# Kernel tuning notes

Hardware: AMD Instinct MI355X
Metric: run time of the kernel (lower is better)

The kernel has to match this reference:

```python
import jax, jax.numpy as jnp
import numpy as np

N_QUBITS = 6      # 4 data + 2 ancilla
N_DATA = 4
N_LAYERS = 4
N_GROUPS = 8
DIM = 2 ** N_QUBITS  # 64 statevector amplitudes (real: RY + CNOT keep state real)
GN_GROUPS = 32
EPS = 1e-5


def _cnot_ring_perm():
    # CNOT(q, q+1 mod n) ring applied sequentially; compose into one basis permutation.
    n = N_QUBITS
    f = np.arange(DIM)
    for c in range(n):
        t = (c + 1) % n
        cbit = (f >> (n - 1 - c)) & 1
        f = np.where(cbit == 1, f ^ (1 << (n - 1 - t)), f)
    # new_state[f[i]] = old_state[i]  =>  new = old[finv]
    finv = np.empty(DIM, dtype=np.int64)
    finv[f] = np.arange(DIM)
    return jnp.asarray(finv)


def _zsign():
    i = np.arange(DIM)[:, None]
    q = np.arange(N_DATA)[None, :]
    return jnp.asarray(1.0 - 2.0 * ((i >> (N_QUBITS - 1 - q)) & 1), dtype=jnp.float32)


PERM = _cnot_ring_perm()
ZSIGN = _zsign()


def _group_norm(x, gamma, beta):
    B, C, H, W = x.shape
    xg = x.reshape(B, GN_GROUPS, C // GN_GROUPS, H, W)
    mu = xg.mean(axis=(2, 3, 4), keepdims=True)
    var = xg.var(axis=(2, 3, 4), keepdims=True)
    xn = ((xg - mu) * jax.lax.rsqrt(var + EPS)).reshape(B, C, H, W)
    return xn * gamma[None, :, None, None] + beta[None, :, None, None]


def _apply_ry(state, half_angle, q):
    # state: [B,H,W,G,64]; half_angle: [B,H,W,G]; RY = [[c,-s],[s,c]] on qubit q
    pre, post = 2 ** q, 2 ** (N_QUBITS - 1 - q)
    s = state.reshape(state.shape[:-1] + (pre, 2, post))
    c = jnp.cos(half_angle)[..., None, None]
    sn = jnp.sin(half_angle)[..., None, None]
    a0, a1 = s[..., 0, :], s[..., 1, :]
    new = jnp.stack([c * a0 - sn * a1, sn * a0 + c * a1], axis=-2)
    return new.reshape(state.shape)


def _forward(x, emb, gamma, beta, w_in, b_in, theta, w_style, b_style, w_out, b_out):
    B, C, H, W = x.shape
    h = _group_norm(x, gamma, beta)                       # norm0
    emb_a = emb * jax.nn.sigmoid(emb)                     # SiLU(emb)
    # 1x1 projection to per-group data-qubit rotation angles: [B,H,W,G,4]
    ang = jnp.einsum('oc,bchw->bohw', w_in, h) + b_in[None, :, None, None]
    ang = ang.reshape(B, N_GROUPS, N_DATA, H, W).transpose(0, 3, 4, 1, 2)
    # style modulation of circuit parameters: [B,G,L,Q]
    style = (emb_a @ w_style.T + b_style).reshape(B, N_GROUPS, N_LAYERS, N_QUBITS)
    # init |0...0> per pixel per group
    state = jnp.zeros((B, H, W, N_GROUPS, DIM), x.dtype).at[..., 0].set(1.0)
    for l in range(N_LAYERS):
        for q in range(N_QUBITS):
            a = theta[:, l, q][None, None, None, :] + style[:, :, l, q][:, None, None, :]
            if q < N_DATA:                                # data reuploading each layer
                a = a + ang[..., q]
            state = _apply_ry(state, 0.5 * a, q)
        state = state[..., PERM]                          # CNOT ring entangler
    probs = state * state
    meas = probs @ ZSIGN                                  # [B,H,W,G,4] <Z> on data qubits
    meas = meas.transpose(0, 3, 4, 1, 2).reshape(B, N_GROUPS * N_DATA, H, W)
    out = jnp.einsum('oc,bchw->bohw', w_out, meas) + b_out[None, :, None, None]
    return out + x                                        # residual


def setup_inputs() -> dict:
    key = jax.random.key(0)
    ks = jax.random.split(key, 6)
    B, C, H, W, E = 16, 256, 32, 32, 512
    return {
        'x': jax.random.normal(ks[0], (B, C, H, W), jnp.float32),
        'emb': jax.random.normal(ks[1], (B, E), jnp.float32),
        'gamma': jnp.ones((C,), jnp.float32),
        'beta': jnp.zeros((C,), jnp.float32),
        'w_in': jax.random.normal(ks[2], (32, C), jnp.float32) * 0.1,
        'b_in': jnp.zeros((32,), jnp.float32),
        'theta': jax.random.normal(ks[3], (N_GROUPS, N_LAYERS, N_QUBITS), jnp.float32) * 0.5,
        'w_style': jax.random.normal(ks[4], (N_GROUPS * N_LAYERS * N_QUBITS, E), jnp.float32) * 0.02,
        'b_style': jnp.zeros((N_GROUPS * N_LAYERS * N_QUBITS,), jnp.float32),
        'w_out': jax.random.normal(ks[5], (C, 32), jnp.float32) * 0.05,
        'b_out': jnp.zeros((C,), jnp.float32),
    }


def reference(x, emb, gamma, beta, w_in, b_in, theta, w_style, b_style, w_out, b_out):
    return _forward(x, emb, gamma, beta, w_in, b_in, theta, w_style, b_style, w_out, b_out)
```

## Files before the change

kernel.cpp:

```cpp
#include <hip/hip_runtime.h>
#include <math.h>

#define NB 16
#define NC 256
#define NHW 1024
#define NE 512
#define NGQ 8
#define NDQ 4
#define NLQ 4
#define NQB 6
#define QDIM 64
#define PIX 32
#define XS_STRIDE 36

struct PermT { int v[QDIM]; };
constexpr PermT make_perm() {
    PermT P{};
    int f[QDIM] = {};
    for (int i = 0; i < QDIM; ++i) f[i] = i;
    for (int c = 0; c < NQB; ++c) {
        int t = (c + 1) % NQB;
        for (int i = 0; i < QDIM; ++i)
            if ((f[i] >> (NQB - 1 - c)) & 1) f[i] ^= 1 << (NQB - 1 - t);
    }
    for (int i = 0; i < QDIM; ++i) P.v[f[i]] = i;
    return P;
}
constexpr PermT PERM = make_perm();

__global__ __launch_bounds__(256) void k_stats(const float* __restrict__ x,
                                               float* __restrict__ mu,
                                               float* __restrict__ rs) {
    int bg = blockIdx.x;
    const float4* xp = (const float4*)(x + (size_t)bg * 8 * NHW);
    float s = 0.f, ss = 0.f;
    for (int i = threadIdx.x; i < 8 * NHW / 4; i += 256) {
        float4 v = xp[i];
        s  += v.x + v.y + v.z + v.w;
        ss += v.x*v.x + v.y*v.y + v.z*v.z + v.w*v.w;
    }
    __shared__ float red0[4], red1[4];
    #pragma unroll
    for (int o = 32; o; o >>= 1) { s += __shfl_down(s, o); ss += __shfl_down(ss, o); }
    int lane = threadIdx.x & 63, w = threadIdx.x >> 6;
    if (lane == 0) { red0[w] = s; red1[w] = ss; }
    __syncthreads();
    if (threadIdx.x == 0) {
        s  = red0[0] + red0[1] + red0[2] + red0[3];
        ss = red1[0] + red1[1] + red1[2] + red1[3];
        float m = s * (1.f / 8192.f);
        float var = ss * (1.f / 8192.f) - m * m;
        mu[bg] = m;
        rs[bg] = rsqrtf(var + 1e-5f);
    }
}

__global__ __launch_bounds__(256) void k_style(const float* __restrict__ emb,
                                               const float* __restrict__ w_style,
                                               const float* __restrict__ b_style,
                                               const float* __restrict__ theta,
                                               float* __restrict__ A) {
    int b = blockIdx.x;
    __shared__ float es[NE];
    int t = threadIdx.x;
    for (int i = t; i < NE; i += 256) {
        float v = emb[b * NE + i];
        es[i] = v / (1.f + __expf(-v));
    }
    __syncthreads();
    int j0 = t >> 3, sub = t & 7;
    for (int pass = 0; pass < 6; ++pass) {
        int j = pass * 32 + j0;
        const float* wr = w_style + (size_t)j * NE + sub * 64;
        const float* er = es + sub * 64;
        float acc = 0.f;
        #pragma unroll
        for (int i = 0; i < 64; i += 4) {
            float4 w4 = *(const float4*)(wr + i);
            acc = fmaf(w4.x, er[i],   acc);
            acc = fmaf(w4.y, er[i+1], acc);
            acc = fmaf(w4.z, er[i+2], acc);
            acc = fmaf(w4.w, er[i+3], acc);
        }
        acc += __shfl_xor(acc, 1);
        acc += __shfl_xor(acc, 2);
        acc += __shfl_xor(acc, 4);
        if (sub == 0) A[b * 192 + j] = theta[j] + b_style[j] + acc;
    }
}

__global__ __launch_bounds__(256, 2) void k_main(const float* __restrict__ x,
                                                 const float* __restrict__ gamma,
                                                 const float* __restrict__ beta,
                                                 const float* __restrict__ w_in,
                                                 const float* __restrict__ b_in,
                                                 const float* __restrict__ A,
                                                 const float* __restrict__ w_out,
                                                 const float* __restrict__ b_out,
                                                 const float* __restrict__ mu,
                                                 const float* __restrict__ rs,
                                                 float* __restrict__ out) {
    __shared__ float xs[NC * XS_STRIDE];
    __shared__ float as_[32 * 32];
    __shared__ float ms[32 * 32];

    int blk = blockIdx.x;
    int b = blk >> 5;
    int pbase = (blk & 31) * PIX;
    int t = threadIdx.x;

    {
        int c0 = t >> 3, f4 = (t & 7) * 4;
        #pragma unroll
        for (int k = 0; k < 8; ++k) {
            int c = c0 + 32 * k;
            int gidx = b * 32 + (c >> 3);
            float m = mu[gidx], r = rs[gidx];
            float sc = r * gamma[c];
            float sh = beta[c] - m * sc;
            float4 x4 = *(const float4*)(x + (size_t)(b * NC + c) * NHW + pbase + f4);
            float4 h4;
            h4.x = fmaf(x4.x, sc, sh);
            h4.y = fmaf(x4.y, sc, sh);
            h4.z = fmaf(x4.z, sc, sh);
            h4.w = fmaf(x4.w, sc, sh);
            *(float4*)(xs + c * XS_STRIDE + f4) = h4;
        }
    }
    __syncthreads();

    {
        int o = t >> 3, f4 = (t & 7) * 4;
        const float* wr = w_in + o * NC;
        float4 acc = {0.f, 0.f, 0.f, 0.f};
        #pragma unroll 4
        for (int c = 0; c < NC; c += 4) {
            float4 w4 = *(const float4*)(wr + c);
            const float* xc = xs + c * XS_STRIDE + f4;
            float4 h0 = *(const float4*)(xc);
            float4 h1 = *(const float4*)(xc + XS_STRIDE);
            float4 h2 = *(const float4*)(xc + 2 * XS_STRIDE);
            float4 h3 = *(const float4*)(xc + 3 * XS_STRIDE);
            acc.x = fmaf(w4.x, h0.x, fmaf(w4.y, h1.x, fmaf(w4.z, h2.x, fmaf(w4.w, h3.x, acc.x))));
            acc.y = fmaf(w4.x, h0.y, fmaf(w4.y, h1.y, fmaf(w4.z, h2.y, fmaf(w4.w, h3.y, acc.y))));
            acc.z = fmaf(w4.x, h0.z, fmaf(w4.y, h1.z, fmaf(w4.z, h2.z, fmaf(w4.w, h3.z, acc.z))));
            acc.w = fmaf(w4.x, h0.w, fmaf(w4.y, h1.w, fmaf(w4.z, h2.w, fmaf(w4.w, h3.w, acc.w))));
        }
        float bi = b_in[o];
        float4 r = {acc.x + bi, acc.y + bi, acc.z + bi, acc.w + bi};
        *(float4*)(as_ + o * 32 + f4) = r;
    }
    __syncthreads();

    {
        int p = t & 31, g = t >> 5;
        float angp[NDQ];
        #pragma unroll
        for (int d = 0; d < NDQ; ++d) angp[d] = as_[(g * NDQ + d) * 32 + p];
        const float* Ab = A + b * 192 + g * 24;

        float st[QDIM];
        #pragma unroll
        for (int i = 0; i < QDIM; ++i) st[i] = 0.f;
        st[0] = 1.f;

        #pragma unroll
        for (int l = 0; l < NLQ; ++l) {
            #pragma unroll
            for (int q = 0; q < NQB; ++q) {
                float a = Ab[l * NQB + q] + (q < NDQ ? angp[q] : 0.f);
                float sn, cs;
                __sincosf(0.5f * a, &sn, &cs);
                const int m = 32 >> q;
                #pragma unroll
                for (int i = 0; i < QDIM; ++i) {
                    if (i & m) continue;
                    float a0 = st[i], a1 = st[i | m];
                    st[i]     = cs * a0 - sn * a1;
                    st[i | m] = sn * a0 + cs * a1;
                }
            }
            float tmp[QDIM];
            #pragma unroll
            for (int i = 0; i < QDIM; ++i) tmp[i] = st[PERM.v[i]];
            #pragma unroll
            for (int i = 0; i < QDIM; ++i) st[i] = tmp[i];
        }

        float pr[QDIM];
        #pragma unroll
        for (int i = 0; i < QDIM; ++i) pr[i] = st[i] * st[i];
        #pragma unroll
        for (int d = 0; d < NDQ; ++d) {
            const int mb = 32 >> d;
            float acc = 0.f;
            #pragma unroll
            for (int i = 0; i < QDIM; ++i) acc += (i & mb) ? -pr[i] : pr[i];
            ms[(g * NDQ + d) * 32 + p] = acc;
        }
    }
    __syncthreads();

    {
        int c0 = t >> 3, f4 = (t & 7) * 4;
        #pragma unroll
        for (int k = 0; k < 8; ++k) {
            int c = c0 + 32 * k;
            const float* wr = w_out + c * 32;
            float4 acc = {0.f, 0.f, 0.f, 0.f};
            #pragma unroll
            for (int o = 0; o < 32; o += 4) {
                float4 w4 = *(const float4*)(wr + o);
                const float* mc = ms + o * 32 + f4;
                float4 m0 = *(const float4*)(mc);
                float4 m1 = *(const float4*)(mc + 32);
                float4 m2 = *(const float4*)(mc + 64);
                float4 m3 = *(const float4*)(mc + 96);
                acc.x = fmaf(w4.x, m0.x, fmaf(w4.y, m1.x, fmaf(w4.z, m2.x, fmaf(w4.w, m3.x, acc.x))));
                acc.y = fmaf(w4.x, m0.y, fmaf(w4.y, m1.y, fmaf(w4.z, m2.y, fmaf(w4.w, m3.y, acc.y))));
                acc.z = fmaf(w4.x, m0.z, fmaf(w4.y, m1.z, fmaf(w4.z, m2.z, fmaf(w4.w, m3.z, acc.z))));
                acc.w = fmaf(w4.x, m0.w, fmaf(w4.y, m1.w, fmaf(w4.z, m2.w, fmaf(w4.w, m3.w, acc.w))));
            }
            size_t gidx = (size_t)(b * NC + c) * NHW + pbase + f4;
            float4 x4 = *(const float4*)(x + gidx);
            float bo = b_out[c];
            float4 r;
            r.x = acc.x + bo + x4.x;
            r.y = acc.y + bo + x4.y;
            r.z = acc.z + bo + x4.z;
            r.w = acc.w + bo + x4.w;
            *(float4*)(out + gidx) = r;
        }
    }
}

extern "C" void kernel_launch(void* const* d_in, const int* in_sizes, int n_in,
                              void* d_out, int out_size, void* d_ws, size_t ws_size,
                              hipStream_t stream) {
    const float* x       = (const float*)d_in[0];
    const float* emb     = (const float*)d_in[1];
    const float* gamma   = (const float*)d_in[2];
    const float* beta    = (const float*)d_in[3];
    const float* w_in    = (const float*)d_in[4];
    const float* b_in    = (const float*)d_in[5];
    const float* theta   = (const float*)d_in[6];
    const float* w_style = (const float*)d_in[7];
    const float* b_style = (const float*)d_in[8];
    const float* w_out   = (const float*)d_in[9];
    const float* b_out   = (const float*)d_in[10];
    float* out = (float*)d_out;

    float* ws = (float*)d_ws;
    float* mu = ws;
    float* rs = ws + 512;
    float* A  = ws + 1024;

    k_stats<<<NB * 32, 256, 0, stream>>>(x, mu, rs);
    k_style<<<NB, 256, 0, stream>>>(emb, w_style, b_style, theta, A);
    k_main<<<NB * 32, 256, 0, stream>>>(x, gamma, beta, w_in, b_in, A,
                                        w_out, b_out, mu, rs, out);
}
```

Before: 141.6 us.

## Transpose shared tiles to pixel-major and pack statevector math into float2 ops

Shared-memory activations are stored pixel-major, so each thread owns one pixel and streams weights as wave-uniform loads in both 1x1 projections. The statevector update is rewritten with two-wide vectors so the compiler can emit packed FMA instructions, and the last-qubit rotation becomes an in-pair swizzle. The measurement reduction is simplified, and the output stage now writes scalar coalesced values per pixel instead of float4. The risks are the scalar global stores and loads in the output stage, and possible LDS bank conflicts from the transposed stores in the normalization stage.

```diff
diff --git a/kernel.cpp b/kernel.cpp
--- a/kernel.cpp
+++ b/kernel.cpp
@@ -5,13 +5,15 @@
 #define NC 256
 #define NHW 1024
 #define NE 512
-#define NGQ 8
 #define NDQ 4
 #define NLQ 4
 #define NQB 6
 #define QDIM 64
 #define PIX 32
-#define XS_STRIDE 36
+#define XPAD 260
+#define MPAD 36
+
+typedef float v2f __attribute__((ext_vector_type(2)));
 
 struct PermT { int v[QDIM]; };
 constexpr PermT make_perm() {
@@ -89,6 +91,8 @@
     }
 }
 
+#define ELEM(arr, j) (((j) & 1) ? arr[(j) >> 1].y : arr[(j) >> 1].x)
+
 __global__ __launch_bounds__(256, 2) void k_main(const float* __restrict__ x,
                                                  const float* __restrict__ gamma,
                                                  const float* __restrict__ beta,
@@ -100,9 +104,9 @@
                                                  const float* __restrict__ mu,
                                                  const float* __restrict__ rs,
                                                  float* __restrict__ out) {
-    __shared__ float xs[NC * XS_STRIDE];
-    __shared__ float as_[32 * 32];
-    __shared__ float ms[32 * 32];
+    __shared__ float xs[PIX * XPAD];
+    __shared__ float as_[PIX * MPAD];
+    __shared__ float ms[PIX * MPAD];
 
     int blk = blockIdx.x;
     int b = blk >> 5;
@@ -119,117 +123,139 @@
             float sc = r * gamma[c];
             float sh = beta[c] - m * sc;
             float4 x4 = *(const float4*)(x + (size_t)(b * NC + c) * NHW + pbase + f4);
-            float4 h4;
-            h4.x = fmaf(x4.x, sc, sh);
-            h4.y = fmaf(x4.y, sc, sh);
-            h4.z = fmaf(x4.z, sc, sh);
-            h4.w = fmaf(x4.w, sc, sh);
-            *(float4*)(xs + c * XS_STRIDE + f4) = h4;
-        }
-    }
-    __syncthreads();
-
-    {
-        int o = t >> 3, f4 = (t & 7) * 4;
-        const float* wr = w_in + o * NC;
-        float4 acc = {0.f, 0.f, 0.f, 0.f};
-        #pragma unroll 4
+            xs[(f4 + 0) * XPAD + c] = fmaf(x4.x, sc, sh);
+            xs[(f4 + 1) * XPAD + c] = fmaf(x4.y, sc, sh);
+            xs[(f4 + 2) * XPAD + c] = fmaf(x4.z, sc, sh);
+            xs[(f4 + 3) * XPAD + c] = fmaf(x4.w, sc, sh);
+        }
+    }
+    __syncthreads();
+
+    {
+        int og = t >> 5, p = t & 31;
+        const float* wbase = w_in + og * 4 * NC;
+        const float* hrow = xs + p * XPAD;
+        float a0 = 0.f, a1 = 0.f, a2 = 0.f, a3 = 0.f;
+        #pragma unroll 8
         for (int c = 0; c < NC; c += 4) {
-            float4 w4 = *(const float4*)(wr + c);
-            const float* xc = xs + c * XS_STRIDE + f4;
-            float4 h0 = *(const float4*)(xc);
-            float4 h1 = *(const float4*)(xc + XS_STRIDE);
-            float4 h2 = *(const float4*)(xc + 2 * XS_STRIDE);
-            float4 h3 = *(const float4*)(xc + 3 * XS_STRIDE);
-            acc.x = fmaf(w4.x, h0.x, fmaf(w4.y, h1.x, fmaf(w4.z, h2.x, fmaf(w4.w, h3.x, acc.x))));
-            acc.y = fmaf(w4.x, h0.y, fmaf(w4.y, h1.y, fmaf(w4.z, h2.y, fmaf(w4.w, h3.y, acc.y))));
-            acc.z = fmaf(w4.x, h0.z, fmaf(w4.y, h1.z, fmaf(w4.z, h2.z, fmaf(w4.w, h3.z, acc.z))));
-            acc.w = fmaf(w4.x, h0.w, fmaf(w4.y, h1.w, fmaf(w4.z, h2.w, fmaf(w4.w, h3.w, acc.w))));
-        }
-        float bi = b_in[o];
-        float4 r = {acc.x + bi, acc.y + bi, acc.z + bi, acc.w + bi};
-        *(float4*)(as_ + o * 32 + f4) = r;
-    }
-    __syncthreads();
-
-    {
-        int p = t & 31, g = t >> 5;
-        float angp[NDQ];
-        #pragma unroll
-        for (int d = 0; d < NDQ; ++d) angp[d] = as_[(g * NDQ + d) * 32 + p];
+            float4 h = *(const float4*)(hrow + c);
+            float4 w0 = *(const float4*)(wbase + c);
+            float4 w1 = *(const float4*)(wbase + NC + c);
+            float4 w2 = *(const float4*)(wbase + 2 * NC + c);
+            float4 w3 = *(const float4*)(wbase + 3 * NC + c);
+            a0 = fmaf(w0.x, h.x, fmaf(w0.y, h.y, fmaf(w0.z, h.z, fmaf(w0.w, h.w, a0))));
+            a1 = fmaf(w1.x, h.x, fmaf(w1.y, h.y, fmaf(w1.z, h.z, fmaf(w1.w, h.w, a1))));
+            a2 = fmaf(w2.x, h.x, fmaf(w2.y, h.y, fmaf(w2.z, h.z, fmaf(w2.w, h.w, a2))));
+            a3 = fmaf(w3.x, h.x, fmaf(w3.y, h.y, fmaf(w3.z, h.z, fmaf(w3.w, h.w, a3))));
+        }
+        float4 bi = *(const float4*)(b_in + og * 4);
+        float4 r = {a0 + bi.x, a1 + bi.y, a2 + bi.z, a3 + bi.w};
+        *(float4*)(as_ + p * MPAD + og * 4) = r;
+    }
+    __syncthreads();
+
+    {
+        int g = t >> 5, p = t & 31;
+        float4 angv = *(const float4*)(as_ + p * MPAD + g * 4);
+        float angp[NDQ] = {angv.x, angv.y, angv.z, angv.w};
         const float* Ab = A + b * 192 + g * 24;
-
-        float st[QDIM];
-        #pragma unroll
-        for (int i = 0; i < QDIM; ++i) st[i] = 0.f;
-        st[0] = 1.f;
+        float Ar[24];
+        #pragma unroll
+        for (int j = 0; j < 24; ++j) Ar[j] = Ab[j];
+
+        v2f st2[QDIM / 2];
+        #pragma unroll
+        for (int k = 0; k < QDIM / 2; ++k) st2[k] = (v2f){0.f, 0.f};
+        st2[0].x = 1.f;
 
         #pragma unroll
         for (int l = 0; l < NLQ; ++l) {
             #pragma unroll
             for (int q = 0; q < NQB; ++q) {
-                float a = Ab[l * NQB + q] + (q < NDQ ? angp[q] : 0.f);
+                float a = Ar[l * NQB + q] + (q < NDQ ? angp[q] : 0.f);
                 float sn, cs;
                 __sincosf(0.5f * a, &sn, &cs);
-                const int m = 32 >> q;
-                #pragma unroll
-                for (int i = 0; i < QDIM; ++i) {
-                    if (i & m) continue;
-                    float a0 = st[i], a1 = st[i | m];
-                    st[i]     = cs * a0 - sn * a1;
-                    st[i | m] = sn * a0 + cs * a1;
+                v2f cs2 = {cs, cs};
+                if (q < 5) {
+                    const int m = 32 >> q;
+                    v2f sn2 = {sn, sn};
+                    #pragma unroll
+                    for (int i = 0; i < QDIM; i += 2) {
+                        if (i & m) continue;
+                        int klo = i >> 1, khi = (i | m) >> 1;
+                        v2f lo = st2[klo], hi = st2[khi];
+                        v2f tm = sn2 * hi;
+                        v2f um = cs2 * hi;
+                        st2[klo] = __builtin_elementwise_fma(cs2, lo, -tm);
+                        st2[khi] = __builtin_elementwise_fma(sn2, lo, um);
+                    }
+                } else {
+                    v2f msn = {-sn, sn};
+                    #pragma unroll
+                    for (int k = 0; k < QDIM / 2; ++k) {
+                        v2f a0 = st2[k];
+                        v2f asw = __builtin_shufflevector(a0, a0, 1, 0);
+                        st2[k] = __builtin_elementwise_fma(msn, asw, cs2 * a0);
+                    }
                 }
             }
-            float tmp[QDIM];
-            #pragma unroll
-            for (int i = 0; i < QDIM; ++i) tmp[i] = st[PERM.v[i]];
-            #pragma unroll
-            for (int i = 0; i < QDIM; ++i) st[i] = tmp[i];
-        }
-
-        float pr[QDIM];
-        #pragma unroll
-        for (int i = 0; i < QDIM; ++i) pr[i] = st[i] * st[i];
-        #pragma unroll
-        for (int d = 0; d < NDQ; ++d) {
-            const int mb = 32 >> d;
+            v2f nst[QDIM / 2];
+            #pragma unroll
+            for (int k = 0; k < QDIM / 2; ++k) {
+                v2f n;
+                n.x = ELEM(st2, PERM.v[2 * k]);
+                n.y = ELEM(st2, PERM.v[2 * k + 1]);
+                nst[k] = n;
+            }
+            #pragma unroll
+            for (int k = 0; k < QDIM / 2; ++k) st2[k] = nst[k];
+        }
+
+        float s4[16];
+        #pragma unroll
+        for (int h = 0; h < 16; ++h) {
+            v2f p0 = st2[2 * h] * st2[2 * h];
+            v2f p1 = st2[2 * h + 1] * st2[2 * h + 1];
+            s4[h] = (p0.x + p0.y) + (p1.x + p1.y);
+        }
+        float meas[NDQ] = {0.f, 0.f, 0.f, 0.f};
+        #pragma unroll
+        for (int h = 0; h < 16; ++h) {
+            #pragma unroll
+            for (int d = 0; d < NDQ; ++d) {
+                if ((h >> (3 - d)) & 1) meas[d] -= s4[h];
+                else                    meas[d] += s4[h];
+            }
+        }
+        float4 mv = {meas[0], meas[1], meas[2], meas[3]};
+        *(float4*)(ms + p * MPAD + g * 4) = mv;
+    }
+    __syncthreads();
+
+    {
+        int cg = t >> 5, p = t & 31;
+        float mreg[32];
+        #pragma unroll
+        for (int j = 0; j < 8; ++j) {
+            float4 m4 = *(const float4*)(ms + p * MPAD + j * 4);
+            mreg[4 * j] = m4.x; mreg[4 * j + 1] = m4.y;
+            mreg[4 * j + 2] = m4.z; mreg[4 * j + 3] = m4.w;
+        }
+        #pragma unroll 4
+        for (int c0 = 0; c0 < 32; ++c0) {
+            int c = cg * 32 + c0;
+            const float* wr = w_out + c * 32;
             float acc = 0.f;
-            #pragma unroll
-            for (int i = 0; i < QDIM; ++i) acc += (i & mb) ? -pr[i] : pr[i];
-            ms[(g * NDQ + d) * 32 + p] = acc;
-        }
-    }
-    __syncthreads();
-
-    {
-        int c0 = t >> 3, f4 = (t & 7) * 4;
-        #pragma unroll
-        for (int k = 0; k < 8; ++k) {
-            int c = c0 + 32 * k;
-            const float* wr = w_out + c * 32;
-            float4 acc = {0.f, 0.f, 0.f, 0.f};
             #pragma unroll
             for (int o = 0; o < 32; o += 4) {
                 float4 w4 = *(const float4*)(wr + o);
-                const float* mc = ms + o * 32 + f4;
-                float4 m0 = *(const float4*)(mc);
-                float4 m1 = *(const float4*)(mc + 32);
-                float4 m2 = *(const float4*)(mc + 64);
-                float4 m3 = *(const float4*)(mc + 96);
-                acc.x = fmaf(w4.x, m0.x, fmaf(w4.y, m1.x, fmaf(w4.z, m2.x, fmaf(w4.w, m3.x, acc.x))));
-                acc.y = fmaf(w4.x, m0.y, fmaf(w4.y, m1.y, fmaf(w4.z, m2.y, fmaf(w4.w, m3.y, acc.y))));
-                acc.z = fmaf(w4.x, m0.z, fmaf(w4.y, m1.z, fmaf(w4.z, m2.z, fmaf(w4.w, m3.z, acc.z))));
-                acc.w = fmaf(w4.x, m0.w, fmaf(w4.y, m1.w, fmaf(w4.z, m2.w, fmaf(w4.w, m3.w, acc.w))));
-            }
-            size_t gidx = (size_t)(b * NC + c) * NHW + pbase + f4;
-            float4 x4 = *(const float4*)(x + gidx);
-            float bo = b_out[c];
-            float4 r;
-            r.x = acc.x + bo + x4.x;
-            r.y = acc.y + bo + x4.y;
-            r.z = acc.z + bo + x4.z;
-            r.w = acc.w + bo + x4.w;
-            *(float4*)(out + gidx) = r;
+                acc = fmaf(w4.x, mreg[o],     acc);
+                acc = fmaf(w4.y, mreg[o + 1], acc);
+                acc = fmaf(w4.z, mreg[o + 2], acc);
+                acc = fmaf(w4.w, mreg[o + 3], acc);
+            }
+            size_t gidx = (size_t)(b * NC + c) * NHW + pbase + p;
+            out[gidx] = acc + b_out[c] + x[gidx];
         }
     }
 }
```

Measured after the change: 150.6 us. +6.4%, slower.
